# Kernel optimization log

Measured on AMD Instinct MI355X. Metric: run time of the kernel, lower is better.

Reference implementation:

```python
import jax, jax.numpy as jnp
import numpy as np
import math

D_EMBED = 1536
N_HEADS = 12
D_AUG = D_EMBED // 3          # 512
HEAD_DIM = D_EMBED // N_HEADS # 128
ROPE_BASE = 10000.0


def apply_rope(x):
    # x: [B, S, H, D], interleaved-pair RoPE (torchtune convention)
    B, S, H, D = x.shape
    half = D // 2
    freqs = 1.0 / (ROPE_BASE ** (jnp.arange(0, D, 2, dtype=jnp.float32) / D))  # [half]
    ang = jnp.arange(S, dtype=jnp.float32)[:, None] * freqs[None, :]           # [S, half]
    cos = jnp.cos(ang)[None, :, None, :]  # [1,S,1,half]
    sin = jnp.sin(ang)[None, :, None, :]
    xr = x.reshape(B, S, H, half, 2)
    x1, x2 = xr[..., 0], xr[..., 1]
    out = jnp.stack([x1 * cos - x2 * sin, x1 * sin + x2 * cos], axis=-1)
    return out.reshape(B, S, H, D).astype(x.dtype)


def setup_inputs() -> dict:
    key = jax.random.key(0)
    ks = jax.random.split(key, 7)
    B, S = 2, 2048
    s = 0.02
    return {
        "q": jax.random.normal(ks[0], (B, S, D_EMBED), jnp.float32),
        "k": jax.random.normal(ks[1], (B, S, D_EMBED), jnp.float32),
        "v": jax.random.normal(ks[2], (B, S, D_EMBED), jnp.float32),
        "W_q": jax.random.normal(ks[3], (D_EMBED, D_EMBED), jnp.float32) * s,
        "W_k": jax.random.normal(ks[4], (D_EMBED, D_EMBED), jnp.float32) * s,
        "W_v": jax.random.normal(ks[5], (D_AUG, D_AUG), jnp.float32) * s,
        "W_o": jax.random.normal(ks[6], (D_EMBED, D_EMBED), jnp.float32) * s,
    }


def reference(q, k, v, W_q, W_k, W_v, W_o):
    # Dropout layers are identity in eval mode.
    B, S, _ = q.shape
    qh = q @ W_q.T                                     # [B,S,D]
    kh = k @ W_k.T
    v_mid = v[:, :, D_AUG:2 * D_AUG] @ W_v.T           # [B,S,D_AUG]
    vh = jnp.concatenate(
        [v_mid, jnp.zeros_like(v_mid), jnp.zeros_like(v_mid)], axis=-1)  # [B,S,D]

    qh = qh.reshape(B, S, N_HEADS, HEAD_DIM)
    kh = kh.reshape(B, S, N_HEADS, HEAD_DIM)
    vh = vh.reshape(B, S, N_HEADS, HEAD_DIM)

    qh = apply_rope(qh)
    kh = apply_rope(kh)

    scores = jnp.einsum('bqhd,bkhd->bhqk', qh, kh) / math.sqrt(HEAD_DIM)
    causal = jnp.triu(jnp.ones((S, S), dtype=bool), k=1)
    scores = jnp.where(causal[None, None], -jnp.inf, scores)
    probs = jax.nn.softmax(scores, axis=-1)

    attn = jnp.einsum('bhqk,bkhd->bqhd', probs, vh).reshape(B, S, D_EMBED)
    return attn @ W_o.T
```

## Files before the change

kernel.cpp:

```cpp
#include <hip/hip_runtime.h>
#include <hip/hip_bf16.h>

typedef __attribute__((ext_vector_type(8))) short short8;
typedef __attribute__((ext_vector_type(4))) short short4v;
typedef __attribute__((ext_vector_type(4))) float f32x4;

__device__ __forceinline__ short f2bf(float f) {
    union { float f; unsigned u; } v; v.f = f;
    unsigned r = (v.u + 0x7fffu + ((v.u >> 16) & 1u)) >> 16;
    return (short)r;
}
__device__ __forceinline__ float bf2f(short s) {
    union { unsigned u; float f; } v; v.u = ((unsigned)(unsigned short)s) << 16;
    return v.f;
}
__device__ __forceinline__ f32x4 zero4() { f32x4 z = {0.f, 0.f, 0.f, 0.f}; return z; }

__device__ __forceinline__ void gl16(const void* g, void* l) {
    __builtin_amdgcn_global_load_lds(
        (const __attribute__((address_space(1))) void*)g,
        (__attribute__((address_space(3))) void*)l, 16, 0, 0);
}

__global__ __launch_bounds__(256) void convertA_kernel(
    const float* __restrict__ q, const float* __restrict__ k,
    const float* __restrict__ Wq, const float* __restrict__ Wk,
    short* __restrict__ qb, short* __restrict__ kb,
    short* __restrict__ Wqb, short* __restrict__ Wkb)
{
    const int e0 = (blockIdx.x * 256 + threadIdx.x) * 8;
    const float* src; short* dst; int n;
    switch (blockIdx.z) {
    case 0:  n = 6291456; src = q + e0;  dst = qb;  break;
    case 1:  n = 6291456; src = k + e0;  dst = kb;  break;
    case 2:  n = 786432;  src = Wq + e0; dst = Wqb; break;
    default: n = 786432;  src = Wk + e0; dst = Wkb; break;
    }
    if (e0 >= n) return;
    float4 f0 = ((const float4*)src)[0];
    float4 f1 = ((const float4*)src)[1];
    short8 o;
    o[0]=f2bf(f0.x); o[1]=f2bf(f0.y); o[2]=f2bf(f0.z); o[3]=f2bf(f0.w);
    o[4]=f2bf(f1.x); o[5]=f2bf(f1.y); o[6]=f2bf(f1.z); o[7]=f2bf(f1.w);
    *(short8*)(dst + e0) = o;
}

template<int MODE>
__device__ __forceinline__ void gemm97_bm64(
    const short* __restrict__ A, const short* __restrict__ B, short* __restrict__ Cp,
    int K, int lda, int ldb, int ldc, short* As, short* Bs)
{
    const int bm = blockIdx.y * 64;
    const int bn = blockIdx.x * 128;
    const int tid = threadIdx.x;
    const int w = tid >> 6;
    const int lane = tid & 63;
    const int l15 = lane & 15;
    const int quad = lane >> 4;
    const int wm = (w >> 1) * 32;
    const int wn = (w & 1) * 64;

    const int srA = w * 16 + (lane >> 2);
    const int srB = w * 32 + (lane >> 2);
    const int sc  = (lane & 3) * 8;
    const short* ga = A + (size_t)(bm + srA) * lda + sc;
    const short* gb = B + (size_t)(bn + srB) * ldb + sc;

    f32x4 acc[2][4];
#pragma unroll
    for (int i = 0; i < 2; i++)
#pragma unroll
        for (int j = 0; j < 4; j++) acc[i][j] = zero4();

    for (int k0 = 0; k0 < K; k0 += 64) {
        __syncthreads();
#pragma unroll
        for (int p = 0; p < 2; p++) {
            gl16(ga + k0 + p * 32,                    &As[p * 2048 + (w * 16) * 32]);
            gl16(gb + k0 + p * 32,                    &Bs[p * 4096 + (w * 32) * 32]);
            gl16(gb + k0 + p * 32 + (size_t)16 * ldb, &Bs[p * 4096 + (w * 32 + 16) * 32]);
        }
        __syncthreads();

        short8 af[2][2], bf[2][4];
#pragma unroll
        for (int p = 0; p < 2; p++) {
#pragma unroll
            for (int i = 0; i < 2; i++)
                af[p][i] = *(const short8*)&As[p * 2048 + (wm + i * 16 + l15) * 32 + quad * 8];
#pragma unroll
            for (int j = 0; j < 4; j++)
                bf[p][j] = *(const short8*)&Bs[p * 4096 + (wn + j * 16 + l15) * 32 + quad * 8];
        }
#pragma unroll
        for (int i = 0; i < 2; i++)
#pragma unroll
            for (int j = 0; j < 4; j++) {
                acc[i][j] = __builtin_amdgcn_mfma_f32_16x16x32_bf16(af[0][i], bf[0][j], acc[i][j], 0, 0, 0);
                acc[i][j] = __builtin_amdgcn_mfma_f32_16x16x32_bf16(af[1][i], bf[1][j], acc[i][j], 0, 0, 0);
            }
    }

#pragma unroll
    for (int i = 0; i < 2; i++)
#pragma unroll
        for (int j = 0; j < 4; j++) {
            const int col = bn + wn + j * 16 + l15;
            const int row0 = bm + wm + i * 16 + quad * 4;
            const int pairi = (col & 127) >> 1;
            const float freq = exp2f(-(float)(2 * pairi) * (13.287712379549449f / 128.0f));
            const bool even = (l15 & 1) == 0;
#pragma unroll
            for (int r = 0; r < 4; r++) {
                const float own = acc[i][j][r];
                const float other = __shfl_xor(own, 1, 64);
                const float pos = (float)((row0 + r) & 2047);
                const float ang = pos * freq;
                const float n = rintf(ang * 0.15915494309189535f);
                const float rr = (ang - n * 6.28125f) - n * 1.9353071795864769e-3f;
                float s, c;
                __sincosf(rr, &s, &c);
                const float x1 = even ? own : other;
                const float x2 = even ? other : own;
                const float res = even ? (x1 * c - x2 * s) : (x1 * s + x2 * c);
                if constexpr (MODE == 1) {
                    Cp[(size_t)(row0 + r) * ldc + col] = f2bf(res);
                } else {
                    const int seq = row0 + r;
                    const int b_ = seq >> 11;
                    const int s2 = seq & 2047;
                    Cp[(size_t)(b_ * 4 + (col >> 7)) * 262144 + (s2 >> 5) * 4096
                       + ((s2 >> 4) & 1) * 2048 + ((col >> 5) & 3) * 512
                       + ((col >> 3) & 3) * 128 + (s2 & 15) * 8 + (col & 7)] = f2bf(res);
                }
            }
        }
}

__device__ __forceinline__ void gemm_f32T_vF(
    const float* __restrict__ A, const float* __restrict__ Bw, short* __restrict__ Cp,
    int K, int lda, int ldb, short* As, short* Bs)
{
    const int bm = blockIdx.y * 64;
    const int bn = blockIdx.x * 128;
    const int tid = threadIdx.x;
    const int w = tid >> 6;
    const int lane = tid & 63;
    const int l15 = lane & 15;
    const int quad = lane >> 4;
    const int wm = (w >> 1) * 32;
    const int wn = (w & 1) * 64;
    const int srA = tid >> 2;
    const int scA = (tid & 3) * 8;
    const int srB = tid >> 1;
    const int scB = (tid & 1) * 16;

    f32x4 acc[2][4];
#pragma unroll
    for (int i = 0; i < 2; i++)
#pragma unroll
        for (int j = 0; j < 4; j++) acc[i][j] = zero4();

    for (int k0 = 0; k0 < K; k0 += 32) {
        __syncthreads();
        {
            const float* src = A + (size_t)(bm + srA) * lda + k0 + scA;
            short* dst = &As[srA * 40 + scA];
            const float4* s4 = (const float4*)src;
            float4 f0 = s4[0], f1 = s4[1];
            short8 t0;
            t0[0]=f2bf(f0.x); t0[1]=f2bf(f0.y); t0[2]=f2bf(f0.z); t0[3]=f2bf(f0.w);
            t0[4]=f2bf(f1.x); t0[5]=f2bf(f1.y); t0[6]=f2bf(f1.z); t0[7]=f2bf(f1.w);
            *(short8*)dst = t0;
        }
        {
            const float* src = Bw + (size_t)(bn + srB) * ldb + k0 + scB;
            short* dst = &Bs[srB * 40 + scB];
            const float4* s4 = (const float4*)src;
            float4 f0 = s4[0], f1 = s4[1], f2 = s4[2], f3 = s4[3];
            short8 t0, t1;
            t0[0]=f2bf(f0.x); t0[1]=f2bf(f0.y); t0[2]=f2bf(f0.z); t0[3]=f2bf(f0.w);
            t0[4]=f2bf(f1.x); t0[5]=f2bf(f1.y); t0[6]=f2bf(f1.z); t0[7]=f2bf(f1.w);
            t1[0]=f2bf(f2.x); t1[1]=f2bf(f2.y); t1[2]=f2bf(f2.z); t1[3]=f2bf(f2.w);
            t1[4]=f2bf(f3.x); t1[5]=f2bf(f3.y); t1[6]=f2bf(f3.z); t1[7]=f2bf(f3.w);
            *(short8*)dst = t0; *(short8*)(dst + 8) = t1;
        }
        __syncthreads();

        short8 af[2], bfr[4];
#pragma unroll
        for (int i = 0; i < 2; i++)
            af[i] = *(const short8*)&As[(wm + i * 16 + l15) * 40 + quad * 8];
#pragma unroll
        for (int j = 0; j < 4; j++)
            bfr[j] = *(const short8*)&Bs[(wn + j * 16 + l15) * 40 + quad * 8];
#pragma unroll
        for (int i = 0; i < 2; i++)
#pragma unroll
            for (int j = 0; j < 4; j++)
                acc[i][j] = __builtin_amdgcn_mfma_f32_16x16x32_bf16(af[i], bfr[j], acc[i][j], 0, 0, 0);
    }

#pragma unroll
    for (int i = 0; i < 2; i++)
#pragma unroll
        for (int j = 0; j < 4; j++) {
            const int col = bn + wn + j * 16 + l15;
            const int row0 = bm + wm + i * 16 + quad * 4;
            const int b_ = row0 >> 11;
            const int s2 = row0 & 2047;
            short4v p;
#pragma unroll
            for (int r = 0; r < 4; r++) p[r] = f2bf(acc[i][j][r]);
            const size_t addr = (size_t)(b_ * 4 + (col >> 7)) * 262144 + (s2 >> 5) * 4096
                              + ((col >> 4) & 7) * 512 + ((s2 >> 3) & 3) * 128
                              + (col & 15) * 8 + (s2 & 7);
            *(short4v*)&Cp[addr] = p;
        }
}

__global__ __launch_bounds__(256) void proj_kernel(
    const short* __restrict__ qb, const short* __restrict__ kb, const float* __restrict__ v,
    const short* __restrict__ Wqb, const short* __restrict__ Wkb, const float* __restrict__ Wv,
    short* __restrict__ qh, short* __restrict__ khF, short* __restrict__ vF)
{
    __shared__ short smem[12288];
    switch (blockIdx.z) {
    case 0:  gemm97_bm64<1>(qb, Wqb, qh,  1536, 1536, 1536, 512, smem, smem + 4096); break;
    case 1:  gemm97_bm64<2>(kb, Wkb, khF, 1536, 1536, 1536, 512, smem, smem + 4096); break;
    default: gemm_f32T_vF(v + 512, Wv, vF, 512, 1536, 512, smem, smem + 2560); break;
    }
}

__global__ __launch_bounds__(256) void outproj_kernel(
    const short* __restrict__ attn, const float* __restrict__ Wo, float* __restrict__ out)
{
    __shared__ short smem[2][5120];
    const int bm = blockIdx.y * 128;
    const int bn = blockIdx.x * 128;
    const int tid = threadIdx.x;
    const int w = tid >> 6;
    const int lane = tid & 63;
    const int l15 = lane & 15;
    const int quad = lane >> 4;
    const int wm = (w >> 1) * 64;
    const int wn = (w & 1) * 64;
    const int srow = tid >> 1;
    const int scol = (tid & 1) * 16;
    short* As = smem[0];
    short* Bs = smem[1];
    const int K = 512, lda = 512, ldb = 1536, ldc = 1536;

    f32x4 acc[4][4];
#pragma unroll
    for (int i = 0; i < 4; i++)
#pragma unroll
        for (int j = 0; j < 4; j++) acc[i][j] = zero4();

    for (int k0 = 0; k0 < K; k0 += 32) {
        __syncthreads();
        {
            const short* src = attn + (size_t)(bm + srow) * lda + k0 + scol;
            short* dst = &As[srow * 40 + scol];
            const uint4* s4 = (const uint4*)src;
            uint4 a = s4[0], b = s4[1];
            *(uint4*)dst = a; *(uint4*)(dst + 8) = b;
        }
        {
            const float* src = Wo + (size_t)(bn + srow) * ldb + k0 + scol;
            short* dst = &Bs[srow * 40 + scol];
            const float4* s4 = (const float4*)src;
            float4 f0 = s4[0], f1 = s4[1], f2 = s4[2], f3 = s4[3];
            short8 t0, t1;
            t0[0]=f2bf(f0.x); t0[1]=f2bf(f0.y); t0[2]=f2bf(f0.z); t0[3]=f2bf(f0.w);
            t0[4]=f2bf(f1.x); t0[5]=f2bf(f1.y); t0[6]=f2bf(f1.z); t0[7]=f2bf(f1.w);
            t1[0]=f2bf(f2.x); t1[1]=f2bf(f2.y); t1[2]=f2bf(f2.z); t1[3]=f2bf(f2.w);
            t1[4]=f2bf(f3.x); t1[5]=f2bf(f3.y); t1[6]=f2bf(f3.z); t1[7]=f2bf(f3.w);
            *(short8*)dst = t0; *(short8*)(dst + 8) = t1;
        }
        __syncthreads();

        short8 af[4], bfr[4];
#pragma unroll
        for (int i = 0; i < 4; i++)
            af[i] = *(const short8*)&As[(wm + i * 16 + l15) * 40 + quad * 8];
#pragma unroll
        for (int j = 0; j < 4; j++)
            bfr[j] = *(const short8*)&Bs[(wn + j * 16 + l15) * 40 + quad * 8];
#pragma unroll
        for (int i = 0; i < 4; i++)
#pragma unroll
            for (int j = 0; j < 4; j++)
                acc[i][j] = __builtin_amdgcn_mfma_f32_16x16x32_bf16(af[i], bfr[j], acc[i][j], 0, 0, 0);
    }

#pragma unroll
    for (int i = 0; i < 4; i++)
#pragma unroll
        for (int j = 0; j < 4; j++) {
            const int col = bn + wn + j * 16 + l15;
            const int row0 = bm + wm + i * 16 + quad * 4;
#pragma unroll
            for (int r = 0; r < 4; r++)
                out[(size_t)(row0 + r) * ldc + col] = acc[i][j][r];
        }
}

__global__ __launch_bounds__(256, 4) void flash_kernel(
    const short* __restrict__ qh, const short* __restrict__ khF,
    const short* __restrict__ vF, short* __restrict__ attn)
{
    __shared__ float Os[4][16][128];
    __shared__ short Ps[4][16 * 40];
    __shared__ float Lp[4][16];

    const int id = blockIdx.x;
    const int hb = id & 7;
    const int b = hb & 1;
    const int h = hb >> 1;
    const int s = id >> 3;
    const int m = s & 31;
    const int g = s >> 5;
    const int base = (g >> 1) * 32 + m;
    const int qt = (g & 1) ? (127 - base) : base;
    const int tid = threadIdx.x;
    const int w = tid >> 6;
    const int lane = tid & 63;
    const int l15 = lane & 15;
    const int quad = lane >> 4;

    const float scale = 0.08838834764831845f;
    const float MFIX = 24.0f;

    const int q0 = qt * 16;
    const int ntiles = (q0 + 47) >> 5;

    const short* qrow = qh + (size_t)(b * 2048 + q0 + l15) * 512 + h * 128;
    short8 aq[4];
#pragma unroll
    for (int kk = 0; kk < 4; kk++)
        aq[kk] = *(const short8*)&qrow[kk * 32 + quad * 8];

    const short* kfb = khF + (size_t)(b * 4 + h) * 262144 + lane * 8;
    const short* vfb = vF  + (size_t)(b * 4 + h) * 262144 + lane * 8;

    f32x4 o[8];
#pragma unroll
    for (int dt = 0; dt < 8; dt++) o[dt] = zero4();
    float lsum[4] = {0.f, 0.f, 0.f, 0.f};

    short* pw = &Ps[w][0];

    for (int t = w; t < ntiles; t += 4) {
        const int kb0 = t * 32;
        const short* kt_ = kfb + t * 4096;
        const short* vt_ = vfb + t * 4096;

        f32x4 sc[2];
#pragma unroll
        for (int ct = 0; ct < 2; ct++) {
            sc[ct] = zero4();
#pragma unroll
            for (int kk = 0; kk < 4; kk++) {
                short8 bk = *(const short8*)&kt_[ct * 2048 + kk * 512];
                sc[ct] = __builtin_amdgcn_mfma_f32_16x16x32_bf16(aq[kk], bk, sc[ct], 0, 0, 0);
            }
        }

        short8 bv[8];
#pragma unroll
        for (int dt = 0; dt < 8; dt++)
            bv[dt] = *(const short8*)&vt_[dt * 512];

        const int rbase = q0 + quad * 4;
        float p[2][4];
#pragma unroll
        for (int ct = 0; ct < 2; ct++) {
            const int kcol = kb0 + ct * 16 + l15;
#pragma unroll
            for (int r = 0; r < 4; r++) {
                const float e = __expf(sc[ct][r] * scale - MFIX);
                const float pv = (kcol > rbase + r) ? 0.0f : e;
                p[ct][r] = pv;
                lsum[r] += pv;
            }
        }

#pragma unroll
        for (int ct = 0; ct < 2; ct++)
#pragma unroll
            for (int r = 0; r < 4; r++)
                pw[(quad * 4 + r) * 40 + ct * 16 + l15] = f2bf(p[ct][r]);
        short8 ap = *(const short8*)&pw[l15 * 40 + quad * 8];

#pragma unroll
        for (int dt = 0; dt < 8; dt++)
            o[dt] = __builtin_amdgcn_mfma_f32_16x16x32_bf16(ap, bv[dt], o[dt], 0, 0, 0);
    }

#pragma unroll
    for (int r = 0; r < 4; r++) {
        float vsum = lsum[r];
#pragma unroll
        for (int off = 1; off < 16; off <<= 1)
            vsum += __shfl_xor(vsum, off, 64);
        if (l15 == 0) Lp[w][quad * 4 + r] = vsum;
#pragma unroll
        for (int dt = 0; dt < 8; dt++)
            Os[w][quad * 4 + r][dt * 16 + l15] = o[dt][r];
    }
    __syncthreads();

    {
        const int row = tid >> 4;
        const int d0 = (tid & 15) * 8;
        const float L = Lp[0][row] + Lp[1][row] + Lp[2][row] + Lp[3][row];
        const float rL = 1.0f / L;
        short8 ov;
#pragma unroll
        for (int j = 0; j < 8; j++) {
            const float osum = Os[0][row][d0 + j] + Os[1][row][d0 + j]
                             + Os[2][row][d0 + j] + Os[3][row][d0 + j];
            ov[j] = f2bf(osum * rL);
        }
        *(short8*)&attn[(size_t)(b * 2048 + q0 + row) * 512 + h * 128 + d0] = ov;
    }
}

extern "C" void kernel_launch(void* const* d_in, const int* in_sizes, int n_in,
                              void* d_out, int out_size, void* d_ws, size_t ws_size,
                              hipStream_t stream) {
    const float* q  = (const float*)d_in[0];
    const float* k  = (const float*)d_in[1];
    const float* v  = (const float*)d_in[2];
    const float* Wq = (const float*)d_in[3];
    const float* Wk = (const float*)d_in[4];
    const float* Wv = (const float*)d_in[5];
    const float* Wo = (const float*)d_in[6];
    float* out = (float*)d_out;

    const size_t MB = 1024 * 1024;
    char* ws = (char*)d_ws;
    short* qh   = (short*)(ws);
    short* khF  = (short*)(ws + 4 * MB);
    short* vF   = (short*)(ws + 8 * MB);
    short* Wqb  = (short*)(ws + 12 * MB);
    short* Wkb  = (short*)(ws + 13 * MB + 512 * 1024);
    short* attn = (short*)(ws + 12 * MB);
    short* qb   = (short*)d_out;
    short* kb   = (short*)((char*)d_out + 12 * MB);

    convertA_kernel<<<dim3(3072, 1, 4), 256, 0, stream>>>(q, k, Wq, Wk, qb, kb, Wqb, Wkb);
    proj_kernel<<<dim3(4, 64, 3), 256, 0, stream>>>(qb, kb, v, Wqb, Wkb, Wv, qh, khF, vF);
    flash_kernel<<<dim3(1024, 1, 1), 256, 0, stream>>>(qh, khF, vF, attn);
    outproj_kernel<<<dim3(12, 32, 1), 256, 0, stream>>>(attn, Wo, out);
}
```

Measured before the change: 222.8 us.

## Pre-swizzle Q/K and weights into MFMA fragment layout and drop LDS staging

The fp32->bf16 conversion kernel now writes q, k, W_q and W_k in a per-16-row, per-32-k fragment order that matches the MFMA operand layout. The Q/K projection GEMM then loads fragments straight from global memory into registers, with no LDS staging or barriers, and uses a remapped 128x64 block tile. The aim is to remove shared-memory traffic and synchronisation from the projection. In exchange, operand reuse across waves now relies on cache hits instead of LDS, and the kernel is locked to hardcoded dimensions.

```diff
diff --git a/kernel.cpp b/kernel.cpp
--- a/kernel.cpp
+++ b/kernel.cpp
@@ -15,12 +15,6 @@
     return v.f;
 }
 __device__ __forceinline__ f32x4 zero4() { f32x4 z = {0.f, 0.f, 0.f, 0.f}; return z; }
-
-__device__ __forceinline__ void gl16(const void* g, void* l) {
-    __builtin_amdgcn_global_load_lds(
-        (const __attribute__((address_space(1))) void*)g,
-        (__attribute__((address_space(3))) void*)l, 16, 0, 0);
-}
 
 __global__ __launch_bounds__(256) void convertA_kernel(
     const float* __restrict__ q, const float* __restrict__ k,
@@ -28,83 +22,75 @@
     short* __restrict__ qb, short* __restrict__ kb,
     short* __restrict__ Wqb, short* __restrict__ Wkb)
 {
-    const int e0 = (blockIdx.x * 256 + threadIdx.x) * 8;
-    const float* src; short* dst; int n;
-    switch (blockIdx.z) {
-    case 0:  n = 6291456; src = q + e0;  dst = qb;  break;
-    case 1:  n = 6291456; src = k + e0;  dst = kb;  break;
-    case 2:  n = 786432;  src = Wq + e0; dst = Wqb; break;
-    default: n = 786432;  src = Wk + e0; dst = Wkb; break;
-    }
-    if (e0 >= n) return;
-    float4 f0 = ((const float4*)src)[0];
-    float4 f1 = ((const float4*)src)[1];
-    short8 o;
-    o[0]=f2bf(f0.x); o[1]=f2bf(f0.y); o[2]=f2bf(f0.z); o[3]=f2bf(f0.w);
-    o[4]=f2bf(f1.x); o[5]=f2bf(f1.y); o[6]=f2bf(f1.z); o[7]=f2bf(f1.w);
-    *(short8*)(dst + e0) = o;
-}
-
-template<int MODE>
-__device__ __forceinline__ void gemm97_bm64(
-    const short* __restrict__ A, const short* __restrict__ B, short* __restrict__ Cp,
-    int K, int lda, int ldb, int ldc, short* As, short* Bs)
-{
-    const int bm = blockIdx.y * 64;
-    const int bn = blockIdx.x * 128;
     const int tid = threadIdx.x;
     const int w = tid >> 6;
     const int lane = tid & 63;
     const int l15 = lane & 15;
     const int quad = lane >> 4;
-    const int wm = (w >> 1) * 32;
-    const int wn = (w & 1) * 64;
-
-    const int srA = w * 16 + (lane >> 2);
-    const int srB = w * 32 + (lane >> 2);
-    const int sc  = (lane & 3) * 8;
-    const short* ga = A + (size_t)(bm + srA) * lda + sc;
-    const short* gb = B + (size_t)(bn + srB) * ldb + sc;
-
-    f32x4 acc[2][4];
-#pragma unroll
-    for (int i = 0; i < 2; i++)
-#pragma unroll
-        for (int j = 0; j < 4; j++) acc[i][j] = zero4();
-
-    for (int k0 = 0; k0 < K; k0 += 64) {
-        __syncthreads();
-#pragma unroll
-        for (int p = 0; p < 2; p++) {
-            gl16(ga + k0 + p * 32,                    &As[p * 2048 + (w * 16) * 32]);
-            gl16(gb + k0 + p * 32,                    &Bs[p * 4096 + (w * 32) * 32]);
-            gl16(gb + k0 + p * 32 + (size_t)16 * ldb, &Bs[p * 4096 + (w * 32 + 16) * 32]);
-        }
-        __syncthreads();
-
-        short8 af[2][2], bf[2][4];
-#pragma unroll
-        for (int p = 0; p < 2; p++) {
-#pragma unroll
-            for (int i = 0; i < 2; i++)
-                af[p][i] = *(const short8*)&As[p * 2048 + (wm + i * 16 + l15) * 32 + quad * 8];
-#pragma unroll
-            for (int j = 0; j < 4; j++)
-                bf[p][j] = *(const short8*)&Bs[p * 4096 + (wn + j * 16 + l15) * 32 + quad * 8];
-        }
-#pragma unroll
-        for (int i = 0; i < 2; i++)
-#pragma unroll
-            for (int j = 0; j < 4; j++) {
-                acc[i][j] = __builtin_amdgcn_mfma_f32_16x16x32_bf16(af[0][i], bf[0][j], acc[i][j], 0, 0, 0);
-                acc[i][j] = __builtin_amdgcn_mfma_f32_16x16x32_bf16(af[1][i], bf[1][j], acc[i][j], 0, 0, 0);
-            }
-    }
-
-#pragma unroll
-    for (int i = 0; i < 2; i++)
-#pragma unroll
-        for (int j = 0; j < 4; j++) {
+    const int f = blockIdx.x * 4 + w;
+    const float* src; short* dst; int nfrag;
+    switch (blockIdx.z) {
+    case 0:  nfrag = 12288; src = q;  dst = qb;  break;
+    case 1:  nfrag = 12288; src = k;  dst = kb;  break;
+    case 2:  nfrag = 1536;  src = Wq; dst = Wqb; break;
+    default: nfrag = 1536;  src = Wk; dst = Wkb; break;
+    }
+    if (f >= nfrag) return;
+    const int r16 = f / 48;
+    const int kt  = f - r16 * 48;
+    const float* s = src + (size_t)(r16 * 16 + l15) * 1536 + kt * 32 + quad * 8;
+    const float4 a = ((const float4*)s)[0];
+    const float4 b = ((const float4*)s)[1];
+    short8 o;
+    o[0]=f2bf(a.x); o[1]=f2bf(a.y); o[2]=f2bf(a.z); o[3]=f2bf(a.w);
+    o[4]=f2bf(b.x); o[5]=f2bf(b.y); o[6]=f2bf(b.z); o[7]=f2bf(b.w);
+    *(short8*)(dst + (size_t)f * 512 + lane * 8) = o;
+}
+
+template<int MODE>
+__device__ __forceinline__ void gemm_frag_direct(
+    const short* __restrict__ Af, const short* __restrict__ Bf, short* __restrict__ Cp)
+{
+    const int flat = blockIdx.x + (blockIdx.y << 2);
+    const int bm = (flat >> 3) * 128;
+    const int bn = (flat & 7) * 64;
+    const int tid = threadIdx.x;
+    const int w = tid >> 6;
+    const int lane = tid & 63;
+    const int l15 = lane & 15;
+    const int quad = lane >> 4;
+    const int wm = (w >> 1) * 64;
+    const int wn = (w & 1) * 32;
+
+    const short* ab = Af + (size_t)((bm + wm) >> 4) * 24576 + lane * 8;
+    const short* bb = Bf + (size_t)((bn + wn) >> 4) * 24576 + lane * 8;
+
+    f32x4 acc[4][2];
+#pragma unroll
+    for (int i = 0; i < 4; i++)
+#pragma unroll
+        for (int j = 0; j < 2; j++) acc[i][j] = zero4();
+
+#pragma unroll 2
+    for (int kt = 0; kt < 48; ++kt) {
+        short8 af[4], bf[2];
+#pragma unroll
+        for (int i = 0; i < 4; i++)
+            af[i] = *(const short8*)(ab + i * 24576 + kt * 512);
+#pragma unroll
+        for (int j = 0; j < 2; j++)
+            bf[j] = *(const short8*)(bb + j * 24576 + kt * 512);
+#pragma unroll
+        for (int i = 0; i < 4; i++)
+#pragma unroll
+            for (int j = 0; j < 2; j++)
+                acc[i][j] = __builtin_amdgcn_mfma_f32_16x16x32_bf16(af[i], bf[j], acc[i][j], 0, 0, 0);
+    }
+
+#pragma unroll
+    for (int i = 0; i < 4; i++)
+#pragma unroll
+        for (int j = 0; j < 2; j++) {
             const int col = bn + wn + j * 16 + l15;
             const int row0 = bm + wm + i * 16 + quad * 4;
             const int pairi = (col & 127) >> 1;
@@ -124,7 +110,7 @@
                 const float x2 = even ? other : own;
                 const float res = even ? (x1 * c - x2 * s) : (x1 * s + x2 * c);
                 if constexpr (MODE == 1) {
-                    Cp[(size_t)(row0 + r) * ldc + col] = f2bf(res);
+                    Cp[(size_t)(row0 + r) * 512 + col] = f2bf(res);
                 } else {
                     const int seq = row0 + r;
                     const int b_ = seq >> 11;
@@ -226,8 +212,8 @@
 {
     __shared__ short smem[12288];
     switch (blockIdx.z) {
-    case 0:  gemm97_bm64<1>(qb, Wqb, qh,  1536, 1536, 1536, 512, smem, smem + 4096); break;
-    case 1:  gemm97_bm64<2>(kb, Wkb, khF, 1536, 1536, 1536, 512, smem, smem + 4096); break;
+    case 0:  gemm_frag_direct<1>(qb, Wqb, qh); break;
+    case 1:  gemm_frag_direct<2>(kb, Wkb, khF); break;
     default: gemm_f32T_vF(v + 512, Wv, vF, 512, 1536, 512, smem, smem + 2560); break;
     }
 }
```

Measured after the change: 231.8 us. 1.04x slower.
